# Optimization experiments

Hardware: AMD Instinct MI355X
Metric: run time of the kernel (lower is better)

Reference implementation:

```python
import jax, jax.numpy as jnp
import numpy as np

# Model constants (from Equilibrium3BConfig + hardcoded MambaBlock args)
D_MODEL = 2560
D_INNER = 5120          # expand=2
N_STATE = 128           # d_state
HEADS = 80              # d_inner // headdim
P_HEAD = 64             # headdim
D_CONV = 4
CONV_DIM = D_INNER + 2 * N_STATE        # 5376 (x, B, C share the conv)
D_IN_PROJ = 2 * D_INNER + 2 * N_STATE + HEADS  # 10576 (z, xBC, dt)
N_EXPERTS = 16
TOP_K = 2
M_INTER = 864
MS_INTER = 1728
EPS = 1e-6


def _rms(x, w, eps=EPS):
    xf = x.astype(jnp.float32)
    xf = xf * jax.lax.rsqrt(jnp.mean(xf * xf, axis=-1, keepdims=True) + eps)
    return w * xf.astype(x.dtype)


def setup_inputs() -> dict:
    key = jax.random.key(0)
    ks = jax.random.split(key, 16)
    b, l = 1, 1024
    s = 0.02  # weight scale, keeps activations sane through the deep block
    return {
        "hidden_states": jax.random.normal(ks[0], (b, l, D_MODEL), jnp.float32),
        "w_in": jax.random.normal(ks[1], (D_MODEL, D_IN_PROJ), jnp.float32) * s,
        "conv_w": jax.random.normal(ks[2], (CONV_DIM, D_CONV), jnp.float32) * s,
        "conv_b": jnp.zeros((CONV_DIM,), jnp.float32),
        "dt_bias": jax.random.normal(ks[3], (HEADS,), jnp.float32) * s,
        "A_log": jax.random.normal(ks[4], (HEADS,), jnp.float32) * s,
        "D": jnp.ones((HEADS,), jnp.float32),
        "mamba_norm_w": jnp.ones((D_INNER,), jnp.float32),
        "w_out": jax.random.normal(ks[5], (D_INNER, D_MODEL), jnp.float32) * s,
        "ln1_w": jnp.ones((D_MODEL,), jnp.float32),
        "ln2_w": jnp.ones((D_MODEL,), jnp.float32),
        "router_w": jax.random.normal(ks[6], (D_MODEL, N_EXPERTS), jnp.float32) * s,
        "we_gate": jax.random.normal(ks[7], (N_EXPERTS, D_MODEL, M_INTER), jnp.float32) * s,
        "we_up": jax.random.normal(ks[8], (N_EXPERTS, D_MODEL, M_INTER), jnp.float32) * s,
        "we_down": jax.random.normal(ks[9], (N_EXPERTS, M_INTER, D_MODEL), jnp.float32) * s,
        "ws_gate": jax.random.normal(ks[10], (D_MODEL, MS_INTER), jnp.float32) * s,
        "ws_up": jax.random.normal(ks[11], (D_MODEL, MS_INTER), jnp.float32) * s,
        "ws_down": jax.random.normal(ks[12], (MS_INTER, D_MODEL), jnp.float32) * s,
    }


def _forward(hidden_states, w_in, conv_w, conv_b, dt_bias, A_log, D, mamba_norm_w,
             w_out, ln1_w, ln2_w, router_w, we_gate, we_up, we_down,
             ws_gate, ws_up, ws_down):
    b, l, d = hidden_states.shape

    # ---- Mamba2 (selective scan) sub-block ----
    residual = hidden_states
    x = _rms(hidden_states, ln1_w)
    zxbcdt = x @ w_in  # [b, l, 10576]
    z, xBC, dt = jnp.split(zxbcdt, [D_INNER, D_INNER + CONV_DIM], axis=-1)

    # depthwise causal conv over (x, B, C) channels, then SiLU
    xBC_t = xBC.transpose(0, 2, 1)  # [b, c, l]
    conv = jax.lax.conv_general_dilated(
        xBC_t, conv_w[:, None, :], (1,), [(D_CONV - 1, 0)],
        feature_group_count=CONV_DIM, dimension_numbers=("NCH", "OIH", "NCH"))
    xBC = jax.nn.silu((conv + conv_b[None, :, None]).transpose(0, 2, 1))
    xs, Bc, Cc = jnp.split(xBC, [D_INNER, D_INNER + N_STATE], axis=-1)

    dt = jax.nn.softplus(dt + dt_bias)          # [b, l, h]
    A = -jnp.exp(A_log)                          # [h]
    xh = xs.reshape(b, l, HEADS, P_HEAD)

    # time-major for scan
    dt_l = dt.transpose(1, 0, 2)                 # [l, b, h]
    xh_l = xh.transpose(1, 0, 2, 3)              # [l, b, h, p]
    B_l = Bc.transpose(1, 0, 2)                  # [l, b, n]
    C_l = Cc.transpose(1, 0, 2)                  # [l, b, n]

    def step(h, inp):
        dt_t, x_t, B_t, C_t = inp
        dA = jnp.exp(dt_t * A)                   # [b, h]
        h = h * dA[..., None, None] + (dt_t[..., None] * x_t)[..., None] * B_t[:, None, None, :]
        y = jnp.einsum("bhpn,bn->bhp", h, C_t)
        return h, y

    h0 = jnp.zeros((b, HEADS, P_HEAD, N_STATE), hidden_states.dtype)
    _, y_l = jax.lax.scan(step, h0, (dt_l, xh_l, B_l, C_l))
    y_l = y_l + D[None, None, :, None] * xh_l    # skip term
    y = y_l.transpose(1, 0, 2, 3).reshape(b, l, D_INNER)
    y = _rms(y * jax.nn.silu(z), mamba_norm_w)   # gated RMSNorm
    hidden = residual + y @ w_out

    # ---- DeepSeekMoE sub-block ----
    residual2 = hidden
    xm = _rms(hidden, ln2_w).reshape(b * l, d)
    logits = xm @ router_w
    probs = jax.nn.softmax(logits.astype(jnp.float32), axis=-1)
    topv, topi = jax.lax.top_k(probs, TOP_K)
    topv = topv / jnp.sum(topv, axis=-1, keepdims=True)  # renormalize top-k
    wdense = jnp.sum(jax.nn.one_hot(topi, N_EXPERTS, dtype=xm.dtype)
                     * topv[..., None].astype(xm.dtype), axis=1)  # [T, E]

    # routed experts (SwiGLU), dense-masked faithful math
    hexp = (jax.nn.silu(jnp.einsum("td,edm->tem", xm, we_gate))
            * jnp.einsum("td,edm->tem", xm, we_up))
    y_routed = jnp.einsum("tem,emd,te->td", hexp, we_down, wdense)

    # shared experts (single fused SwiGLU MLP)
    y_shared = (jax.nn.silu(xm @ ws_gate) * (xm @ ws_up)) @ ws_down

    moe = (y_routed + y_shared).reshape(b, l, d)
    return residual2 + moe


def reference(hidden_states, w_in, conv_w, conv_b, dt_bias, A_log, D, mamba_norm_w,
              w_out, ln1_w, ln2_w, router_w, we_gate, we_up, we_down,
              ws_gate, ws_up, ws_down):
    return _forward(hidden_states, w_in, conv_w, conv_b, dt_bias, A_log, D,
                    mamba_norm_w, w_out, ln1_w, ln2_w, router_w,
                    we_gate, we_up, we_down, ws_gate, ws_up, ws_down)
```

## Files before the change

### kernel.cpp

```cpp
#include <hip/hip_runtime.h>

typedef __attribute__((ext_vector_type(4))) float f32x4;
typedef __attribute__((ext_vector_type(8))) __bf16 bf16x8;
typedef __attribute__((ext_vector_type(4))) __bf16 bf16x4;
typedef __attribute__((ext_vector_type(8))) _Float16 f16x8;
typedef __attribute__((ext_vector_type(4))) _Float16 f16x4;

#define D_MODEL 2560
#define D_INNER 5120
#define N_STATE 128
#define HEADS 80
#define P_HEAD 64
#define CONV_DIM 5376
#define D_INPROJ 10576
#define SEQ 1024
#define NCHUNK 16
#define QCHUNK 64
#define NEXP 16
#define M_INTER 864
#define MS_INTER 1728
#define NSLOT 2048
#define NSLOTP 2176

__device__ __forceinline__ float siluf(float x) { return x / (1.f + __expf(-x)); }

__device__ __forceinline__ int swz_p(int k4, int P) {
  return (k4 & ~31) | ((((k4 >> 3) & 3) ^ P) << 3) | (k4 & 7);
}

__device__ __forceinline__ void gl16(const __bf16* g, __bf16* l) {
  __builtin_amdgcn_global_load_lds((const __attribute__((address_space(1))) unsigned int*)g,
                                   (__attribute__((address_space(3))) unsigned int*)l, 16, 0, 0);
}

__device__ __forceinline__ float block_sum256(float v, float* red) {
#pragma unroll
  for (int m = 32; m > 0; m >>= 1) v += __shfl_xor(v, m, 64);
  int w = threadIdx.x >> 6;
  if ((threadIdx.x & 63) == 0) red[w] = v;
  __syncthreads();
  return red[0] + red[1] + red[2] + red[3];
}

template <bool FP16>
__global__ __launch_bounds__(256) void k_rmsnorm_p(const float* __restrict__ in,
                                                   const float* __restrict__ w,
                                                   float* __restrict__ f32out,
                                                   __bf16* __restrict__ ph,
                                                   __bf16* __restrict__ pdh,
                                                   __bf16* __restrict__ pdl, int D) {
  __shared__ float red[4];
  int t = blockIdx.x, tid = threadIdx.x;
  const float* x = in + (size_t)t * D;
  int nd4 = D >> 2;
  float ss = 0.f;
  for (int i = tid; i < nd4; i += 256) {
    float4 v = ((const float4*)x)[i];
    ss += v.x * v.x + v.y * v.y + v.z * v.z + v.w * v.w;
  }
  float tot = block_sum256(ss, red);
  float r = rsqrtf(tot / (float)D + 1e-6f);
  int P = (t >> 1) & 3;
  for (int i = tid; i < nd4; i += 256) {
    float4 v = ((const float4*)x)[i];
    float4 wv = ((const float4*)w)[i];
    float4 o;
    o.x = wv.x * v.x * r; o.y = wv.y * v.y * r; o.z = wv.z * v.z * r; o.w = wv.w * v.w * r;
    if (f32out) ((float4*)(f32out + (size_t)t * D))[i] = o;
    int p = swz_p(i * 4, P);
    if constexpr (FP16) {
      f16x4 hv;
      hv[0] = (_Float16)o.x; hv[1] = (_Float16)o.y; hv[2] = (_Float16)o.z; hv[3] = (_Float16)o.w;
      *(f16x4*)&ph[(size_t)t * D + p] = hv;
    } else {
      bf16x4 hv;
      hv[0] = (__bf16)o.x; hv[1] = (__bf16)o.y; hv[2] = (__bf16)o.z; hv[3] = (__bf16)o.w;
      *(bf16x4*)&ph[(size_t)t * D + p] = hv;
    }
    if (pdh) {
      bf16x4 hv, lv;
      hv[0] = (__bf16)o.x; hv[1] = (__bf16)o.y; hv[2] = (__bf16)o.z; hv[3] = (__bf16)o.w;
      lv[0] = (__bf16)(o.x - (float)hv[0]); lv[1] = (__bf16)(o.y - (float)hv[1]);
      lv[2] = (__bf16)(o.z - (float)hv[2]); lv[3] = (__bf16)(o.w - (float)hv[3]);
      *(bf16x4*)&pdh[(size_t)t * D + p] = hv;
      *(bf16x4*)&pdl[(size_t)t * D + p] = lv;
    }
  }
}

template <bool SPLIT, bool FP16>
__global__ __launch_bounds__(256) void k_transW(const float* __restrict__ W, int ld, int K, int N,
                                                __bf16* __restrict__ Th, __bf16* __restrict__ Tl) {
  __shared__ float T[64][65];
  const int n0 = blockIdx.x * 64, k0 = blockIdx.y * 64, tid = threadIdx.x;
#pragma unroll
  for (int i = 0; i < 16; i++) {
    int idx = tid + i * 256;
    int k = idx >> 6, n = idx & 63;
    float v = 0.f;
    if (n0 + n < N) v = W[(size_t)(k0 + k) * ld + n0 + n];
    T[k][n] = v;
  }
  __syncthreads();
#pragma unroll
  for (int i = 0; i < 4; i++) {
    int idx = tid + i * 256;
    int n = idx >> 4, p4 = (idx & 15) * 4;
    int nn = n0 + n;
    int P = (nn >> 1) & 3;
    if constexpr (SPLIT) {
      bf16x4 hv, lv;
#pragma unroll
      for (int e = 0; e < 4; e++) {
        int p = p4 + e;
        int kk = (p & ~31) | ((((p >> 3) & 3) ^ P) << 3) | (p & 7);
        float v = T[kk][n];
        __bf16 h = (__bf16)v;
        hv[e] = h;
        lv[e] = (__bf16)(v - (float)h);
      }
      *(bf16x4*)&Th[(size_t)nn * K + k0 + p4] = hv;
      *(bf16x4*)&Tl[(size_t)nn * K + k0 + p4] = lv;
    } else if constexpr (FP16) {
      f16x4 hv;
#pragma unroll
      for (int e = 0; e < 4; e++) {
        int p = p4 + e;
        int kk = (p & ~31) | ((((p >> 3) & 3) ^ P) << 3) | (p & 7);
        hv[e] = (_Float16)T[kk][n];
      }
      *(f16x4*)&Th[(size_t)nn * K + k0 + p4] = hv;
    } else {
      bf16x4 hv;
#pragma unroll
      for (int e = 0; e < 4; e++) {
        int p = p4 + e;
        int kk = (p & ~31) | ((((p >> 3) & 3) ^ P) << 3) | (p & 7);
        hv[e] = (__bf16)T[kk][n];
      }
      *(bf16x4*)&Th[(size_t)nn * K + k0 + p4] = hv;
    }
  }
}

template <bool SPLIT, bool FP16>
__global__ __launch_bounds__(256) void k_gemm2(const __bf16* __restrict__ Ah,
                                               const __bf16* __restrict__ Al,
                                               const __bf16* __restrict__ Bh,
                                               const __bf16* __restrict__ Bl,
                                               float* __restrict__ C,
                                               int M, int N, int K, int ks, int nst) {
  constexpr int NP = SPLIT ? 4 : 2;
  __shared__ __bf16 lds[NP * 4096];
  __bf16* const AsH = lds;
  __bf16* const BsH = lds + (SPLIT ? 2 : 1) * 4096;
  __bf16* const AsL = SPLIT ? (lds + 4096) : nullptr;
  __bf16* const BsL = SPLIT ? (lds + 3 * 4096) : nullptr;

  const int tid = threadIdx.x;
  const int T = gridDim.x * gridDim.y * gridDim.z;
  const int linear = blockIdx.x + gridDim.x * (blockIdx.y + gridDim.y * blockIdx.z);
  const int s_idx = (linear & 7) * (T >> 3) + (linear >> 3);
  const int bm = s_idx & 7;
  const int g = s_idx >> 3;
  const int bn = g % gridDim.y;
  const int z = g / gridDim.y;

  const int m0 = bm * 128, n0 = bn * 128;
  const int s0 = (int)(((long long)z * nst) / ks);
  const int s1 = (int)(((long long)(z + 1) * nst) / ks);
  float* __restrict__ Cp = C + (size_t)z * M * N;

  const int lane = tid & 63, wid = tid >> 6;
  const int wr = wid >> 1, wc = wid & 1;
  const int l16 = lane & 15, kl = lane >> 4;

  const int srow = tid >> 2;
  const int schunk = (tid & 3) * 8;
  const size_t aB0 = (size_t)(m0 + srow) * K + schunk;
  const size_t aB1 = aB0 + (size_t)64 * K;
  const size_t bB0 = (size_t)(n0 + srow) * K + schunk;
  const size_t bB1 = bB0 + (size_t)64 * K;
  __bf16* const lA0 = AsH + tid * 8;
  __bf16* const lA1 = AsH + (tid + 256) * 8;
  __bf16* const lB0 = BsH + tid * 8;
  __bf16* const lB1 = BsH + (tid + 256) * 8;

  int aoff[4], boff[4];
#pragma unroll
  for (int mi = 0; mi < 4; mi++) {
    int r = wr * 64 + mi * 16 + l16;
    aoff[mi] = r * 64 + ((kl ^ ((r >> 1) & 3)) << 4);
  }
#pragma unroll
  for (int ni = 0; ni < 4; ni++) {
    int r = wc * 64 + ni * 16 + l16;
    boff[ni] = r * 64 + ((kl ^ ((r >> 1) & 3)) << 4);
  }

  f32x4 acc[4][4];
#pragma unroll
  for (int mi = 0; mi < 4; mi++)
#pragma unroll
    for (int ni = 0; ni < 4; ni++) acc[mi][ni] = f32x4{0.f, 0.f, 0.f, 0.f};

  for (int s = s0; s < s1; ++s) {
    const int k0 = s << 5;
    __syncthreads();
    gl16(Ah + aB0 + k0, lA0);
    gl16(Ah + aB1 + k0, lA1);
    gl16(Bh + bB0 + k0, lB0);
    gl16(Bh + bB1 + k0, lB1);
    if constexpr (SPLIT) {
      gl16(Al + aB0 + k0, AsL + tid * 8);
      gl16(Al + aB1 + k0, AsL + (tid + 256) * 8);
      gl16(Bl + bB0 + k0, BsL + tid * 8);
      gl16(Bl + bB1 + k0, BsL + (tid + 256) * 8);
    }
    __syncthreads();
    if constexpr (!SPLIT && FP16) {
      f16x8 ah[4], bh[4];
#pragma unroll
      for (int mi = 0; mi < 4; mi++) ah[mi] = *(const f16x8*)((const char*)AsH + aoff[mi]);
#pragma unroll
      for (int ni = 0; ni < 4; ni++) bh[ni] = *(const f16x8*)((const char*)BsH + boff[ni]);
#pragma unroll
      for (int mi = 0; mi < 4; mi++)
#pragma unroll
        for (int ni = 0; ni < 4; ni++)
          acc[mi][ni] = __builtin_amdgcn_mfma_f32_16x16x32_f16(ah[mi], bh[ni], acc[mi][ni], 0, 0, 0);
    } else {
      bf16x8 ah[4], bh[4];
#pragma unroll
      for (int mi = 0; mi < 4; mi++) ah[mi] = *(const bf16x8*)((const char*)AsH + aoff[mi]);
#pragma unroll
      for (int ni = 0; ni < 4; ni++) bh[ni] = *(const bf16x8*)((const char*)BsH + boff[ni]);
#pragma unroll
      for (int mi = 0; mi < 4; mi++)
#pragma unroll
        for (int ni = 0; ni < 4; ni++)
          acc[mi][ni] = __builtin_amdgcn_mfma_f32_16x16x32_bf16(ah[mi], bh[ni], acc[mi][ni], 0, 0, 0);
      if constexpr (SPLIT) {
        bf16x8 al[4], bl[4];
#pragma unroll
        for (int mi = 0; mi < 4; mi++) al[mi] = *(const bf16x8*)((const char*)AsL + aoff[mi]);
#pragma unroll
        for (int ni = 0; ni < 4; ni++) bl[ni] = *(const bf16x8*)((const char*)BsL + boff[ni]);
#pragma unroll
        for (int mi = 0; mi < 4; mi++)
#pragma unroll
          for (int ni = 0; ni < 4; ni++) {
            acc[mi][ni] = __builtin_amdgcn_mfma_f32_16x16x32_bf16(ah[mi], bl[ni], acc[mi][ni], 0, 0, 0);
            acc[mi][ni] = __builtin_amdgcn_mfma_f32_16x16x32_bf16(al[mi], bh[ni], acc[mi][ni], 0, 0, 0);
          }
      }
    }
  }
#pragma unroll
  for (int mi = 0; mi < 4; mi++)
#pragma unroll
    for (int ni = 0; ni < 4; ni++)
#pragma unroll
      for (int r = 0; r < 4; r++) {
        int row = m0 + wr * 64 + mi * 16 + kl * 4 + r;
        int col = n0 + wc * 64 + ni * 16 + l16;
        if (col < N) Cp[(size_t)row * N + col] = acc[mi][ni][r];
      }
}

template <bool RES>
__global__ void k_reduce(const float* __restrict__ Pp, int np, int n4,
                         const float* __restrict__ res, float* __restrict__ out) {
  int i = blockIdx.x * 256 + threadIdx.x;
  int stride = gridDim.x * 256;
  for (; i < n4; i += stride) {
    float4 a = ((const float4*)Pp)[i];
    for (int z = 1; z < np; z++) {
      float4 b = ((const float4*)Pp)[(size_t)z * n4 + i];
      a.x += b.x; a.y += b.y; a.z += b.z; a.w += b.w;
    }
    if constexpr (RES) {
      float4 r0 = ((const float4*)res)[i];
      a.x += r0.x; a.y += r0.y; a.z += r0.z; a.w += r0.w;
    }
    ((float4*)out)[i] = a;
  }
}

__global__ void k_dtfin(const float* __restrict__ dtP, const float* __restrict__ dt_bias,
                        const float* __restrict__ A_log, float* __restrict__ dtp,
                        float* __restrict__ dtA) {
  int t = blockIdx.x, h = threadIdx.x;
  if (h < HEADS) {
    float v = dt_bias[h];
#pragma unroll
    for (int z = 0; z < 8; z++) v += dtP[((size_t)z * SEQ + t) * 80 + h];
    float sp = fmaxf(v, 0.f) + log1pf(expf(-fabsf(v)));
    dtp[t * HEADS + h] = sp;
    dtA[t * HEADS + h] = sp * (-expf(A_log[h]));
  }
}

__global__ __launch_bounds__(256) void k_gatherA(const float* __restrict__ xm,
                                                 const int* __restrict__ perm,
                                                 __bf16* __restrict__ Aslots) {
  int s = blockIdx.x, tid = threadIdx.x;
  int t = perm[s];
// ... 98 lines not shown
      if (more) {
#pragma unroll
        for (int e4 = 0; e4 < 4; e4++) {
          bf16x4 h;
          h[0] = (__bf16)nv[0][e4]; h[1] = (__bf16)nv[1][e4];
          h[2] = (__bf16)nv[2][e4]; h[3] = (__bf16)nv[3][e4];
          *(bf16x4*)&Bsl[cur ^ 1][cb * 4 + e4][kb * 4] = h;
        }
      }
      __syncthreads();
      cur ^= 1;
    }
#pragma unroll
    for (int mi = 0; mi < 4; mi++)
#pragma unroll
      for (int ni = 0; ni < 4; ni++)
#pragma unroll
        for (int r = 0; r < 4; r++) {
          int rl = bm * 128 + wr * 64 + mi * 16 + kl * 4 + r;
          int col = n0 + wc * 64 + ni * 16 + l16;
          if (rl < cnt && col < N) Cpl[(size_t)(base + rl) * N + col] = acc[mi][ni][r];
        }
  }
}

__global__ __launch_bounds__(256) void k_silumulE(const float* __restrict__ gP,
                                                  const float* __restrict__ uP,
                                                  const float* __restrict__ slotw,
                                                  __bf16* __restrict__ outp) {
  int s = blockIdx.x, tid = threadIdx.x;
  float w = slotw[s];
  int P = (s >> 1) & 3;
  const size_t PL = (size_t)NSLOTP * M_INTER;
  for (int i = tid; i < M_INTER / 4; i += 256) {
    f32x4 g = f32x4{0.f, 0.f, 0.f, 0.f}, u = f32x4{0.f, 0.f, 0.f, 0.f};
#pragma unroll
    for (int z = 0; z < 4; z++) {
      g += *(const f32x4*)&gP[z * PL + (size_t)s * M_INTER + i * 4];
      u += *(const f32x4*)&uP[z * PL + (size_t)s * M_INTER + i * 4];
    }
    int p = swz_p(i * 4, P);
    bf16x4 h;
    h[0] = (__bf16)(siluf(g[0]) * u[0] * w);
    h[1] = (__bf16)(siluf(g[1]) * u[1] * w);
    h[2] = (__bf16)(siluf(g[2]) * u[2] * w);
    h[3] = (__bf16)(siluf(g[3]) * u[3] * w);
    *(bf16x4*)&outp[(size_t)s * M_INTER + p] = h;
  }
}

__global__ __launch_bounds__(256) void k_silumul_sh2(const float* __restrict__ P4,
                                                     __bf16* __restrict__ outp) {
  int t = blockIdx.x, tid = threadIdx.x;
  int P = (t >> 1) & 3;
  const size_t PL = (size_t)SEQ * 3456;
  for (int i = tid; i < MS_INTER / 4; i += 256) {
    f32x4 g = f32x4{0.f, 0.f, 0.f, 0.f}, u = f32x4{0.f, 0.f, 0.f, 0.f};
#pragma unroll
    for (int z = 0; z < 4; z++) {
      g += *(const f32x4*)&P4[z * PL + (size_t)t * 3456 + i * 4];
      u += *(const f32x4*)&P4[z * PL + (size_t)t * 3456 + 1728 + i * 4];
    }
    int p = swz_p(i * 4, P);
    bf16x4 h;
    h[0] = (__bf16)(siluf(g[0]) * u[0]);
    h[1] = (__bf16)(siluf(g[1]) * u[1]);
    h[2] = (__bf16)(siluf(g[2]) * u[2]);
    h[3] = (__bf16)(siluf(g[3]) * u[3]);
    *(bf16x4*)&outp[(size_t)t * MS_INTER + p] = h;
  }
}

__global__ void k_conv(const float* __restrict__ zx, const float* __restrict__ cw,
                       const float* __restrict__ cb, float* __restrict__ xBC) {
  int cidx = blockIdx.x * 256 + threadIdx.x;
  int t = blockIdx.y;
  if (cidx < CONV_DIM) {
    float acc = cb[cidx];
#pragma unroll
    for (int j = 0; j < 4; j++) {
      int tt = t - 3 + j;
      if (tt >= 0) acc += zx[(size_t)tt * D_INPROJ + D_INNER + cidx] * cw[cidx * 4 + j];
    }
    xBC[(size_t)t * CONV_DIM + cidx] = siluf(acc);
  }
}

__global__ __launch_bounds__(256) void k_scan_intra(
    const float* __restrict__ xBC, const float* __restrict__ dtp,
    const float* __restrict__ dtA, float* __restrict__ y, float* __restrict__ S,
    float* __restrict__ cumA, float* __restrict__ Atot) {
  __shared__ float Bs[64][132];
  __shared__ float Cs[64][132];
  __shared__ float Xs[64][68];
  __shared__ float Gs[64][65];
  __shared__ float da_s[64], a_s[64], dt_sh[64], w_sh[64];
  int c = blockIdx.x, h = blockIdx.y, tid = threadIdx.x;
  int t0 = c * QCHUNK;
#pragma unroll
  for (int i = 0; i < 8; i++) {
    int id = tid + 256 * i;
    int r = id >> 5, c4 = (id & 31) * 4;
    *(float4*)&Bs[r][c4] = *(const float4*)&xBC[(size_t)(t0 + r) * CONV_DIM + D_INNER + c4];
    *(float4*)&Cs[r][c4] = *(const float4*)&xBC[(size_t)(t0 + r) * CONV_DIM + D_INNER + N_STATE + c4];
  }
#pragma unroll
  for (int i = 0; i < 4; i++) {
    int id = tid + 256 * i;
    int r = id >> 4, p4 = (id & 15) * 4;
    *(float4*)&Xs[r][p4] = *(const float4*)&xBC[(size_t)(t0 + r) * CONV_DIM + h * P_HEAD + p4];
  }
  if (tid < 64) {
    da_s[tid] = dtA[(size_t)(t0 + tid) * HEADS + h];
    dt_sh[tid] = dtp[(size_t)(t0 + tid) * HEADS + h];
  }
  __syncthreads();
  if (tid < 64) {
    float a = 0.f;
    for (int i = 0; i <= tid; i++) a += da_s[i];
    a_s[tid] = a;
    cumA[((size_t)c * HEADS + h) * 64 + tid] = a;
  }
  __syncthreads();
  if (tid < 64) {
    w_sh[tid] = __expf(a_s[63] - a_s[tid]) * dt_sh[tid];
    if (tid == 0) Atot[c * HEADS + h] = a_s[63];
  }
  __syncthreads();
  {
    int tq = tid >> 4, sq = tid & 15;
    float gacc[4][4];
#pragma unroll
    for (int j = 0; j < 4; j++)
#pragma unroll
      for (int jj = 0; jj < 4; jj++) gacc[j][jj] = 0.f;
// ... 75 lines not shown
__global__ __launch_bounds__(256) void k_scan_inter(
    const float* __restrict__ xBC, const float* __restrict__ Hin,
    const float* __restrict__ cumA, const float* __restrict__ Dv,
    float* __restrict__ y) {
  __shared__ float Hs[64][132];
  __shared__ float Cs[64][132];
  __shared__ float a_l[64];
  int c = blockIdx.x, h = blockIdx.y, tid = threadIdx.x;
  int t0 = c * QCHUNK;
#pragma unroll
  for (int i = 0; i < 8; i++) {
    int id = tid + 256 * i;
    int r = id >> 5, n4 = (id & 31) * 4;
    *(float4*)&Hs[r][n4] = *(const float4*)&Hin[(((size_t)(c * HEADS + h) * 64 + r) << 7) + n4];
    *(float4*)&Cs[r][n4] = *(const float4*)&xBC[(size_t)(t0 + r) * CONV_DIM + D_INNER + N_STATE + n4];
  }
  if (tid < 64) a_l[tid] = cumA[((size_t)c * HEADS + h) * 64 + tid];
  __syncthreads();
  float Dh = Dv[h];
  int tq = tid >> 4, pq = tid & 15;
  float4 acc[4];
#pragma unroll
  for (int j = 0; j < 4; j++) acc[j] = float4{0.f, 0.f, 0.f, 0.f};
  for (int n4 = 0; n4 < 128; n4 += 4) {
    float4 hv[4], cv[4];
#pragma unroll
    for (int jj = 0; jj < 4; jj++) hv[jj] = *(const float4*)&Hs[pq * 4 + jj][n4];
#pragma unroll
    for (int j = 0; j < 4; j++) cv[j] = *(const float4*)&Cs[tq * 4 + j][n4];
#pragma unroll
    for (int j = 0; j < 4; j++) {
      acc[j].x += cv[j].x * hv[0].x + cv[j].y * hv[0].y + cv[j].z * hv[0].z + cv[j].w * hv[0].w;
      acc[j].y += cv[j].x * hv[1].x + cv[j].y * hv[1].y + cv[j].z * hv[1].z + cv[j].w * hv[1].w;
      acc[j].z += cv[j].x * hv[2].x + cv[j].y * hv[2].y + cv[j].z * hv[2].z + cv[j].w * hv[2].w;
      acc[j].w += cv[j].x * hv[3].x + cv[j].y * hv[3].y + cv[j].z * hv[3].z + cv[j].w * hv[3].w;
    }
  }
#pragma unroll
  for (int j = 0; j < 4; j++) {
    int t = tq * 4 + j;
    float e = __expf(a_l[t]);
    float4 xv = *(const float4*)&xBC[(size_t)(t0 + t) * CONV_DIM + h * P_HEAD + pq * 4];
    size_t yoff = (size_t)(t0 + t) * D_INNER + h * P_HEAD + pq * 4;
    float4 yv = *(float4*)&y[yoff];
    yv.x += e * acc[j].x + Dh * xv.x;
    yv.y += e * acc[j].y + Dh * xv.y;
    yv.z += e * acc[j].z + Dh * xv.z;
    yv.w += e * acc[j].w + Dh * xv.w;
    *(float4*)&y[yoff] = yv;
  }
}

__global__ __launch_bounds__(256) void k_gatednorm_p(const float* __restrict__ y,
                                                     const float* __restrict__ zx,
                                                     const float* __restrict__ w,
                                                     __bf16* __restrict__ ph) {
  __shared__ float vbuf[D_INNER];
  __shared__ float red[4];
  int t = blockIdx.x, tid = threadIdx.x;
  float ss = 0.f;
  for (int i = tid; i < D_INNER / 4; i += 256) {
    float4 yv = *(const float4*)&y[(size_t)t * D_INNER + i * 4];
    float4 zv = *(const float4*)&zx[(size_t)t * D_INPROJ + i * 4];
    float4 v;
    v.x = yv.x * siluf(zv.x); v.y = yv.y * siluf(zv.y);
    v.z = yv.z * siluf(zv.z); v.w = yv.w * siluf(zv.w);
    *(float4*)&vbuf[i * 4] = v;
    ss += v.x * v.x + v.y * v.y + v.z * v.z + v.w * v.w;
  }
  float tot = block_sum256(ss, red);
  float r = rsqrtf(tot / (float)D_INNER + 1e-6f);
  int P = (t >> 1) & 3;
  for (int i = tid; i < D_INNER / 4; i += 256) {
    float4 v = *(const float4*)&vbuf[i * 4];
    float4 wv = *(const float4*)&w[i * 4];
    float4 o;
    o.x = wv.x * v.x * r; o.y = wv.y * v.y * r; o.z = wv.z * v.z * r; o.w = wv.w * v.w * r;
    int p = swz_p(i * 4, P);
    f16x4 hv;
    hv[0] = (_Float16)o.x; hv[1] = (_Float16)o.y; hv[2] = (_Float16)o.z; hv[3] = (_Float16)o.w;
    *(f16x4*)&ph[(size_t)t * D_INNER + p] = hv;
  }
}

__global__ void k_zero(int* counts, int* cursor) {
  int i = threadIdx.x;
  if (i < NEXP) { counts[i] = 0; cursor[i] = 0; }
}

__global__ __launch_bounds__(256) void k_router(const float* __restrict__ xm,
                                                const float* __restrict__ Wr,
                                                int* __restrict__ top_i,
                                                float* __restrict__ top_v,
                                                int* __restrict__ counts) {
  __shared__ float part[16][17];
  __shared__ float lg[16];
  int t = blockIdx.x, tid = threadIdx.x;
  int e = tid & 15, seg = tid >> 4;
  const float* xr = xm + (size_t)t * D_MODEL;
  float s = 0.f;
  for (int i = 0; i < 160; i++) {
    int k = seg * 160 + i;
    s += xr[k] * Wr[(size_t)k * NEXP + e];
  }
  part[seg][e] = s;
  __syncthreads();
  if (tid < 16) {
    float l = 0.f;
    for (int g = 0; g < 16; g++) l += part[g][tid];
    lg[tid] = l;
  }
  __syncthreads();
  if (tid == 0) {
    float mx = lg[0];
    for (int i = 1; i < 16; i++) mx = fmaxf(mx, lg[i]);
    float pe[16];
    for (int i = 0; i < 16; i++) pe[i] = expf(lg[i] - mx);
    int i0 = 0; float v0 = pe[0];
    for (int i = 1; i < 16; i++) if (pe[i] > v0) { v0 = pe[i]; i0 = i; }
    int i1 = -1; float v1 = -1.f;
    for (int i = 0; i < 16; i++) if (i != i0 && pe[i] > v1) { v1 = pe[i]; i1 = i; }
    float inv = 1.f / (v0 + v1);
    top_i[t * 2] = i0; top_i[t * 2 + 1] = i1;
    top_v[t * 2] = v0 * inv; top_v[t * 2 + 1] = v1 * inv;
    atomicAdd(&counts[i0], 1);
    atomicAdd(&counts[i1], 1);
  }
}

__global__ void k_offsets(const int* counts, int* offs, int* cursor) {
  if (threadIdx.x == 0) {
// ... 16 lines not shown
    }
  }
}

__global__ void k_final2(const float* __restrict__ hidden, const float* __restrict__ sh,
                         const float* __restrict__ dsP, const int* __restrict__ slotOf,
                         float* __restrict__ out) {
  int t = blockIdx.y;
  int d4 = (blockIdx.x * 256 + threadIdx.x) * 4;
  if (d4 < D_MODEL) {
    int s0 = slotOf[t * 2], s1 = slotOf[t * 2 + 1];
    f32x4 a = *(const f32x4*)&hidden[(size_t)t * D_MODEL + d4];
    f32x4 b = *(const f32x4*)&sh[(size_t)t * D_MODEL + d4];
    f32x4 acc = a + b;
    const size_t PL = (size_t)NSLOTP * D_MODEL;
#pragma unroll
    for (int z = 0; z < 3; z++) {
      acc += *(const f32x4*)&dsP[z * PL + (size_t)s0 * D_MODEL + d4];
      acc += *(const f32x4*)&dsP[z * PL + (size_t)s1 * D_MODEL + d4];
    }
    *(f32x4*)&out[(size_t)t * D_MODEL + d4] = acc;
  }
}

extern "C" void kernel_launch(void* const* d_in, const int* in_sizes, int n_in,
                              void* d_out, int out_size, void* d_ws, size_t ws_size,
                              hipStream_t stream) {
  const float* hs = (const float*)d_in[0];
  const float* w_in = (const float*)d_in[1];
  const float* conv_w = (const float*)d_in[2];
  const float* conv_b = (const float*)d_in[3];
  const float* dt_bias = (const float*)d_in[4];
  const float* A_log = (const float*)d_in[5];
  const float* Dv = (const float*)d_in[6];
  const float* mnw = (const float*)d_in[7];
  const float* w_out = (const float*)d_in[8];
  const float* ln1 = (const float*)d_in[9];
  const float* ln2 = (const float*)d_in[10];
  const float* router_w = (const float*)d_in[11];
  const float* we_gate = (const float*)d_in[12];
  const float* we_up = (const float*)d_in[13];
  const float* we_down = (const float*)d_in[14];
  const float* ws_gate = (const float*)d_in[15];
  const float* ws_up = (const float*)d_in[16];
  const float* ws_down = (const float*)d_in[17];

  char* base = (char*)d_ws;
  size_t off = 0;
  auto A = [&](size_t bytes) -> void* {
    void* p = base + off;
    off += (bytes + 255) & ~(size_t)255;
    return p;
  };
  float* zx = (float*)A((size_t)SEQ * D_INPROJ * 4);
  float* xbc = (float*)A((size_t)SEQ * CONV_DIM * 4);
  float* xmf = (float*)A((size_t)SEQ * D_MODEL * 4);
  float* dtp = (float*)A((size_t)SEQ * HEADS * 4);
  float* dtA = (float*)A((size_t)SEQ * HEADS * 4);
  float* yf = (float*)A((size_t)SEQ * D_INNER * 4);
  float* cumA = (float*)A((size_t)NCHUNK * HEADS * 64 * 4);
  float* Atot = (float*)A((size_t)NCHUNK * HEADS * 4);
  float* Sbuf = (float*)A((size_t)NCHUNK * HEADS * 64 * 128 * 4);
  float* hidden = (float*)A((size_t)SEQ * D_MODEL * 4);
  float* shout = (float*)A((size_t)SEQ * D_MODEL * 4);
  float* top_v = (float*)A(8192);
  float* slotw = (float*)A(8192);
  int* top_i = (int*)A(8192);
  int* counts = (int*)A(64);
  int* offs = (int*)A(64);
  int* cursor = (int*)A(64);
  int* perm = (int*)A(8192);
  int* slotOf = (int*)A(8192);
  __bf16* xp_h = (__bf16*)A((size_t)SEQ * D_MODEL * 2);
  __bf16* ybp_h = (__bf16*)A((size_t)SEQ * D_INNER * 2);
  __bf16* gbuf_bh = (__bf16*)A((size_t)SEQ * MS_INTER * 2);
  char* REG = (char*)A((size_t)146000000);

  __bf16* winT_h = (__bf16*)REG;
  __bf16* woutT_h = (__bf16*)REG;
  float* partials = (float*)(REG + 60000000);
  __bf16* xdt_h = (__bf16*)(REG + 110000000);
  __bf16* xdt_l = (__bf16*)(REG + 115500000);
  __bf16* wdt_h = (__bf16*)(REG + 121000000);
  __bf16* wdt_l = (__bf16*)(REG + 122000000);
  float* dtP = (float*)(REG + 123000000);
  __bf16* guT = (__bf16*)REG;
  __bf16* downT = (__bf16*)(REG + 18350080);
  float* partials4 = (float*)(REG + 30000000);
  __bf16* Aslots = (__bf16*)REG;
  __bf16* gsl = (__bf16*)(REG + 12000000);
  float* gateP = (float*)(REG + 16000000);
  float* upP = (float*)(REG + 47000000);
  float* dslotsP = (float*)(REG + 78000000);

  k_rmsnorm_p<true><<<SEQ, 256, 0, stream>>>(hs, ln1, nullptr, xp_h, xdt_h, xdt_l, D_MODEL);
  k_transW<false, true><<<dim3(166, 40), 256, 0, stream>>>(w_in, D_INPROJ, D_MODEL, D_INPROJ,
                                                           winT_h, nullptr);
  k_transW<true, false><<<dim3(2, 40), 256, 0, stream>>>(w_in + 10496, D_INPROJ, D_MODEL, 80,
                                                         wdt_h, wdt_l);
  k_gemm2<false, true><<<dim3(8, 83, 1), 256, 0, stream>>>(xp_h, nullptr, winT_h, nullptr, zx,
                                                           SEQ, D_INPROJ, D_MODEL, 1, 80);
  k_gemm2<true, false><<<dim3(8, 1, 8), 256, 0, stream>>>(xdt_h, xdt_l, wdt_h, wdt_l, dtP,
                                                          SEQ, 80, D_MODEL, 8, 80);
  k_dtfin<<<SEQ, 128, 0, stream>>>(dtP, dt_bias, A_log, dtp, dtA);
  k_conv<<<dim3(21, SEQ), 256, 0, stream>>>(zx, conv_w, conv_b, xbc);
  k_scan_intra<<<dim3(NCHUNK, HEADS), 256, 0, stream>>>(xbc, dtp, dtA, yf, Sbuf, cumA, Atot);
  k_scan_state<<<2560, 256, 0, stream>>>(Sbuf, Atot);
  k_scan_inter<<<dim3(NCHUNK, HEADS), 256, 0, stream>>>(xbc, Sbuf, cumA, Dv, yf);
  k_gatednorm_p<<<SEQ, 256, 0, stream>>>(yf, zx, mnw, ybp_h);
  k_transW<false, true><<<dim3(40, 80), 256, 0, stream>>>(w_out, D_MODEL, D_INNER, D_MODEL,
                                                          woutT_h, nullptr);
  k_gemm2<false, true><<<dim3(8, 20, 4), 256, 0, stream>>>(ybp_h, nullptr, woutT_h, nullptr,
                                                           partials, SEQ, D_MODEL, D_INNER, 4, 160);
  k_reduce<true><<<2048, 256, 0, stream>>>(partials, 4, SEQ * D_MODEL / 4, hs, hidden);

  k_rmsnorm_p<false><<<SEQ, 256, 0, stream>>>(hidden, ln2, xmf, xp_h, nullptr, nullptr, D_MODEL);
  k_zero<<<1, 64, 0, stream>>>(counts, cursor);
  k_router<<<SEQ, 256, 0, stream>>>(xmf, router_w, top_i, top_v, counts);
  k_offsets<<<1, 32, 0, stream>>>(counts, offs, cursor);
  k_scatter<<<4, 256, 0, stream>>>(top_i, top_v, cursor, perm, slotOf, slotw);

  k_transW<false, false><<<dim3(27, 40), 256, 0, stream>>>(ws_gate, MS_INTER, D_MODEL, MS_INTER,
                                                           guT, nullptr);
  k_transW<false, false><<<dim3(27, 40), 256, 0, stream>>>(ws_up, MS_INTER, D_MODEL, MS_INTER,
                                                           guT + (size_t)MS_INTER * D_MODEL, nullptr);
  k_gemm2<false, false><<<dim3(8, 27, 4), 256, 0, stream>>>(xp_h, nullptr, guT, nullptr, partials4,
                                                            SEQ, 3456, D_MODEL, 4, 80);
  k_silumul_sh2<<<SEQ, 256, 0, stream>>>(partials4, gbuf_bh);
  k_transW<false, false><<<dim3(40, 27), 256, 0, stream>>>(ws_down, D_MODEL, MS_INTER, D_MODEL,
                                                           downT, nullptr);
  k_gemm2<false, false><<<dim3(8, 20, 4), 256, 0, stream>>>(gbuf_bh, nullptr, downT, nullptr,
                                                            partials4, SEQ, D_MODEL, MS_INTER, 4, 54);
  k_reduce<false><<<2048, 256, 0, stream>>>(partials4, 4, SEQ * D_MODEL / 4, nullptr, shout);

  k_gatherA<<<NSLOT, 256, 0, stream>>>(xmf, perm, Aslots);
  k_gemmE2<4><<<dim3(7, 4, NEXP), 256, 0, stream>>>(Aslots, we_gate, gateP, offs, counts,
                                                    M_INTER, D_MODEL, (long long)D_MODEL * M_INTER);
  k_gemmE2<4><<<dim3(7, 4, NEXP), 256, 0, stream>>>(Aslots, we_up, upP, offs, counts,
                                                    M_INTER, D_MODEL, (long long)D_MODEL * M_INTER);
  k_silumulE<<<NSLOT, 256, 0, stream>>>(gateP, upP, slotw, gsl);
  k_gemmE2<3><<<dim3(20, 3, NEXP), 256, 0, stream>>>(gsl, we_down, dslotsP, offs, counts,
                                                     D_MODEL, M_INTER, (long long)M_INTER * D_MODEL);

  k_final2<<<dim3(3, SEQ), 256, 0, stream>>>(hidden, shout, dslotsP, slotOf, (float*)d_out);
}
```

Baseline: 845.7 us.

## Use BK=64 GEMM tiles with 8-way swizzle and split-K the in-projection

```diff
diff --git a/kernel.cpp b/kernel.cpp
--- a/kernel.cpp
+++ b/kernel.cpp
@@ -27,6 +27,9 @@
 __device__ __forceinline__ int swz_p(int k4, int P) {
   return (k4 & ~31) | ((((k4 >> 3) & 3) ^ P) << 3) | (k4 & 7);
 }
+__device__ __forceinline__ int swz64(int k4, int row) {
+  return (k4 & ~63) | (((((k4 >> 3) & 7) ^ (row & 7)) << 3)) | (k4 & 7);
+}
 
 __device__ __forceinline__ void gl16(const __bf16* g, __bf16* l) {
   __builtin_amdgcn_global_load_lds((const __attribute__((address_space(1))) unsigned int*)g,
@@ -67,17 +70,18 @@
     float4 o;
     o.x = wv.x * v.x * r; o.y = wv.y * v.y * r; o.z = wv.z * v.z * r; o.w = wv.w * v.w * r;
     if (f32out) ((float4*)(f32out + (size_t)t * D))[i] = o;
-    int p = swz_p(i * 4, P);
+    int p64 = swz64(i * 4, t);
     if constexpr (FP16) {
       f16x4 hv;
       hv[0] = (_Float16)o.x; hv[1] = (_Float16)o.y; hv[2] = (_Float16)o.z; hv[3] = (_Float16)o.w;
-      *(f16x4*)&ph[(size_t)t * D + p] = hv;
+      *(f16x4*)&ph[(size_t)t * D + p64] = hv;
     } else {
       bf16x4 hv;
       hv[0] = (__bf16)o.x; hv[1] = (__bf16)o.y; hv[2] = (__bf16)o.z; hv[3] = (__bf16)o.w;
-      *(bf16x4*)&ph[(size_t)t * D + p] = hv;
+      *(bf16x4*)&ph[(size_t)t * D + p64] = hv;
     }
     if (pdh) {
+      int p = swz_p(i * 4, P);
       bf16x4 hv, lv;
       hv[0] = (__bf16)o.x; hv[1] = (__bf16)o.y; hv[2] = (__bf16)o.z; hv[3] = (__bf16)o.w;
       lv[0] = (__bf16)(o.x - (float)hv[0]); lv[1] = (__bf16)(o.y - (float)hv[1]);
@@ -107,8 +111,8 @@
     int idx = tid + i * 256;
     int n = idx >> 4, p4 = (idx & 15) * 4;
     int nn = n0 + n;
-    int P = (nn >> 1) & 3;
     if constexpr (SPLIT) {
+      int P = (nn >> 1) & 3;
       bf16x4 hv, lv;
 #pragma unroll
       for (int e = 0; e < 4; e++) {
@@ -126,7 +130,7 @@
 #pragma unroll
       for (int e = 0; e < 4; e++) {
         int p = p4 + e;
-        int kk = (p & ~31) | ((((p >> 3) & 3) ^ P) << 3) | (p & 7);
+        int kk = swz64(p, nn);
         hv[e] = (_Float16)T[kk][n];
       }
       *(f16x4*)&Th[(size_t)nn * K + k0 + p4] = hv;
@@ -135,7 +139,7 @@
 #pragma unroll
       for (int e = 0; e < 4; e++) {
         int p = p4 + e;
-        int kk = (p & ~31) | ((((p >> 3) & 3) ^ P) << 3) | (p & 7);
+        int kk = swz64(p, nn);
         hv[e] = (__bf16)T[kk][n];
       }
       *(bf16x4*)&Th[(size_t)nn * K + k0 + p4] = hv;
@@ -143,19 +147,24 @@
   }
 }
 
-template <bool SPLIT, bool FP16>
+template <bool SPLIT, bool FP16, int BK>
 __global__ __launch_bounds__(256) void k_gemm2(const __bf16* __restrict__ Ah,
                                                const __bf16* __restrict__ Al,
                                                const __bf16* __restrict__ Bh,
                                                const __bf16* __restrict__ Bl,
                                                float* __restrict__ C,
                                                int M, int N, int K, int ks, int nst) {
-  constexpr int NP = SPLIT ? 4 : 2;
-  __shared__ __bf16 lds[NP * 4096];
+  constexpr int PLE = 128 * BK;
+  constexpr int NPL = SPLIT ? 4 : 2;
+  constexpr int CALLS = PLE / 2048;
+  constexpr int CPR = BK / 8;
+  constexpr int RPC = 256 / CPR;
+  constexpr int KSUB = BK / 32;
+  __shared__ __bf16 lds[NPL * PLE];
   __bf16* const AsH = lds;
-  __bf16* const BsH = lds + (SPLIT ? 2 : 1) * 4096;
-  __bf16* const AsL = SPLIT ? (lds + 4096) : nullptr;
-  __bf16* const BsL = SPLIT ? (lds + 3 * 4096) : nullptr;
+  __bf16* const BsH = lds + (SPLIT ? 2 : 1) * PLE;
+  __bf16* const AsL = SPLIT ? (lds + PLE) : nullptr;
+  __bf16* const BsL = SPLIT ? (lds + 3 * PLE) : nullptr;
 
   const int tid = threadIdx.x;
   const int T = gridDim.x * gridDim.y * gridDim.z;
@@ -175,27 +184,30 @@
   const int wr = wid >> 1, wc = wid & 1;
   const int l16 = lane & 15, kl = lane >> 4;
 
-  const int srow = tid >> 2;
-  const int schunk = (tid & 3) * 8;
-  const size_t aB0 = (size_t)(m0 + srow) * K + schunk;
-  const size_t aB1 = aB0 + (size_t)64 * K;
-  const size_t bB0 = (size_t)(n0 + srow) * K + schunk;
-  const size_t bB1 = bB0 + (size_t)64 * K;
-  __bf16* const lA0 = AsH + tid * 8;
-  __bf16* const lA1 = AsH + (tid + 256) * 8;
-  __bf16* const lB0 = BsH + tid * 8;
-  __bf16* const lB1 = BsH + (tid + 256) * 8;
-
-  int aoff[4], boff[4];
+  const int srow = tid / CPR;
+  const int schunk = (tid % CPR) * 8;
+  size_t aB[CALLS], bB[CALLS];
+#pragma unroll
+  for (int i = 0; i < CALLS; i++) {
+    aB[i] = (size_t)(m0 + srow + RPC * i) * K + schunk;
+    bB[i] = (size_t)(n0 + srow + RPC * i) * K + schunk;
+  }
+
+  int aoff[4][KSUB], boff[4][KSUB];
 #pragma unroll
   for (int mi = 0; mi < 4; mi++) {
-    int r = wr * 64 + mi * 16 + l16;
-    aoff[mi] = r * 64 + ((kl ^ ((r >> 1) & 3)) << 4);
-  }
-#pragma unroll
-  for (int ni = 0; ni < 4; ni++) {
-    int r = wc * 64 + ni * 16 + l16;
-    boff[ni] = r * 64 + ((kl ^ ((r >> 1) & 3)) << 4);
+    int ra = wr * 64 + mi * 16 + l16;
+    int rb = wc * 64 + mi * 16 + l16;
+#pragma unroll
+    for (int kk = 0; kk < KSUB; kk++) {
+      if constexpr (BK == 32) {
+        aoff[mi][kk] = ra * 64 + ((kl ^ ((ra >> 1) & 3)) << 4);
+        boff[mi][kk] = rb * 64 + ((kl ^ ((rb >> 1) & 3)) << 4);
+      } else {
+        aoff[mi][kk] = ra * (2 * BK) + (((kk * 4 + kl) ^ (ra & 7)) << 4);
+        boff[mi][kk] = rb * (2 * BK) + (((kk * 4 + kl) ^ (rb & 7)) << 4);
+      }
+    }
   }
 
   f32x4 acc[4][4];
@@ -205,54 +217,56 @@
     for (int ni = 0; ni < 4; ni++) acc[mi][ni] = f32x4{0.f, 0.f, 0.f, 0.f};
 
   for (int s = s0; s < s1; ++s) {
-    const int k0 = s << 5;
+    const int kof = s * BK;
     __syncthreads();
-    gl16(Ah + aB0 + k0, lA0);
-    gl16(Ah + aB1 + k0, lA1);
-    gl16(Bh + bB0 + k0, lB0);
-    gl16(Bh + bB1 + k0, lB1);
-    if constexpr (SPLIT) {
-      gl16(Al + aB0 + k0, AsL + tid * 8);
-      gl16(Al + aB1 + k0, AsL + (tid + 256) * 8);
-      gl16(Bl + bB0 + k0, BsL + tid * 8);
-      gl16(Bl + bB1 + k0, BsL + (tid + 256) * 8);
+#pragma unroll
+    for (int i = 0; i < CALLS; i++) {
+      gl16(Ah + aB[i] + kof, AsH + (tid + i * 256) * 8);
+      gl16(Bh + bB[i] + kof, BsH + (tid + i * 256) * 8);
+      if constexpr (SPLIT) {
+        gl16(Al + aB[i] + kof, AsL + (tid + i * 256) * 8);
+        gl16(Bl + bB[i] + kof, BsL + (tid + i * 256) * 8);
+      }
     }
     __syncthreads();
-    if constexpr (!SPLIT && FP16) {
-      f16x8 ah[4], bh[4];
-#pragma unroll
-      for (int mi = 0; mi < 4; mi++) ah[mi] = *(const f16x8*)((const char*)AsH + aoff[mi]);
-#pragma unroll
-      for (int ni = 0; ni < 4; ni++) bh[ni] = *(const f16x8*)((const char*)BsH + boff[ni]);
-#pragma unroll
-      for (int mi = 0; mi < 4; mi++)
-#pragma unroll
-        for (int ni = 0; ni < 4; ni++)
-          acc[mi][ni] = __builtin_amdgcn_mfma_f32_16x16x32_f16(ah[mi], bh[ni], acc[mi][ni], 0, 0, 0);
-    } else {
-      bf16x8 ah[4], bh[4];
-#pragma unroll
-      for (int mi = 0; mi < 4; mi++) ah[mi] = *(const bf16x8*)((const char*)AsH + aoff[mi]);
-#pragma unroll
-      for (int ni = 0; ni < 4; ni++) bh[ni] = *(const bf16x8*)((const char*)BsH + boff[ni]);
-#pragma unroll
-      for (int mi = 0; mi < 4; mi++)
-#pragma unroll
-        for (int ni = 0; ni < 4; ni++)
-          acc[mi][ni] = __builtin_amdgcn_mfma_f32_16x16x32_bf16(ah[mi], bh[ni], acc[mi][ni], 0, 0, 0);
-      if constexpr (SPLIT) {
-        bf16x8 al[4], bl[4];
-#pragma unroll
-        for (int mi = 0; mi < 4; mi++) al[mi] = *(const bf16x8*)((const char*)AsL + aoff[mi]);
-#pragma unroll
-        for (int ni = 0; ni < 4; ni++) bl[ni] = *(const bf16x8*)((const char*)BsL + boff[ni]);
+#pragma unroll
+    for (int kk = 0; kk < KSUB; kk++) {
+      if constexpr (!SPLIT && FP16) {
+        f16x8 ah[4], bh[4];
+#pragma unroll
+        for (int mi = 0; mi < 4; mi++) ah[mi] = *(const f16x8*)((const char*)AsH + aoff[mi][kk]);
+#pragma unroll
+        for (int ni = 0; ni < 4; ni++) bh[ni] = *(const f16x8*)((const char*)BsH + boff[ni][kk]);
 #pragma unroll
         for (int mi = 0; mi < 4; mi++)
 #pragma unroll
-          for (int ni = 0; ni < 4; ni++) {
-            acc[mi][ni] = __builtin_amdgcn_mfma_f32_16x16x32_bf16(ah[mi], bl[ni], acc[mi][ni], 0, 0, 0);
-            acc[mi][ni] = __builtin_amdgcn_mfma_f32_16x16x32_bf16(al[mi], bh[ni], acc[mi][ni], 0, 0, 0);
-          }
+          for (int ni = 0; ni < 4; ni++)
+            acc[mi][ni] = __builtin_amdgcn_mfma_f32_16x16x32_f16(ah[mi], bh[ni], acc[mi][ni], 0, 0, 0);
+      } else {
+        bf16x8 ah[4], bh[4];
+#pragma unroll
+        for (int mi = 0; mi < 4; mi++) ah[mi] = *(const bf16x8*)((const char*)AsH + aoff[mi][kk]);
+#pragma unroll
+        for (int ni = 0; ni < 4; ni++) bh[ni] = *(const bf16x8*)((const char*)BsH + boff[ni][kk]);
+#pragma unroll
+        for (int mi = 0; mi < 4; mi++)
+#pragma unroll
+          for (int ni = 0; ni < 4; ni++)
+            acc[mi][ni] = __builtin_amdgcn_mfma_f32_16x16x32_bf16(ah[mi], bh[ni], acc[mi][ni], 0, 0, 0);
+        if constexpr (SPLIT) {
+          bf16x8 al[4], bl[4];
+#pragma unroll
+          for (int mi = 0; mi < 4; mi++) al[mi] = *(const bf16x8*)((const char*)AsL + aoff[mi][kk]);
+#pragma unroll
+          for (int ni = 0; ni < 4; ni++) bl[ni] = *(const bf16x8*)((const char*)BsL + boff[ni][kk]);
+#pragma unroll
+          for (int mi = 0; mi < 4; mi++)
+#pragma unroll
+            for (int ni = 0; ni < 4; ni++) {
+              acc[mi][ni] = __builtin_amdgcn_mfma_f32_16x16x32_bf16(ah[mi], bl[ni], acc[mi][ni], 0, 0, 0);
+              acc[mi][ni] = __builtin_amdgcn_mfma_f32_16x16x32_bf16(al[mi], bh[ni], acc[mi][ni], 0, 0, 0);
+            }
+        }
       }
     }
   }
@@ -457,7 +471,6 @@
 __global__ __launch_bounds__(256) void k_silumul_sh2(const float* __restrict__ P4,
                                                      __bf16* __restrict__ outp) {
   int t = blockIdx.x, tid = threadIdx.x;
-  int P = (t >> 1) & 3;
   const size_t PL = (size_t)SEQ * 3456;
   for (int i = tid; i < MS_INTER / 4; i += 256) {
     f32x4 g = f32x4{0.f, 0.f, 0.f, 0.f}, u = f32x4{0.f, 0.f, 0.f, 0.f};
@@ -466,7 +479,7 @@
       g += *(const f32x4*)&P4[z * PL + (size_t)t * 3456 + i * 4];
       u += *(const f32x4*)&P4[z * PL + (size_t)t * 3456 + 1728 + i * 4];
     }
-    int p = swz_p(i * 4, P);
+    int p = swz64(i * 4, t);
     bf16x4 h;
     h[0] = (__bf16)(siluf(g[0]) * u[0]);
     h[1] = (__bf16)(siluf(g[1]) * u[1]);
@@ -476,8 +489,9 @@
   }
 }
 
-__global__ void k_conv(const float* __restrict__ zx, const float* __restrict__ cw,
-                       const float* __restrict__ cb, float* __restrict__ xBC) {
+__global__ void k_conv(const float* __restrict__ zx0, const float* __restrict__ zx1,
+                       const float* __restrict__ cw, const float* __restrict__ cb,
+                       float* __restrict__ xBC) {
   int cidx = blockIdx.x * 256 + threadIdx.x;
   int t = blockIdx.y;
   if (cidx < CONV_DIM) {
@@ -485,7 +499,10 @@
 #pragma unroll
     for (int j = 0; j < 4; j++) {
       int tt = t - 3 + j;
-      if (tt >= 0) acc += zx[(size_t)tt * D_INPROJ + D_INNER + cidx] * cw[cidx * 4 + j];
+      if (tt >= 0) {
+        size_t idx = (size_t)tt * D_INPROJ + D_INNER + cidx;
+        acc += (zx0[idx] + zx1[idx]) * cw[cidx * 4 + j];
+      }
     }
     xBC[(size_t)t * CONV_DIM + cidx] = siluf(acc);
   }
@@ -667,7 +684,8 @@
 }
 
 __global__ __launch_bounds__(256) void k_gatednorm_p(const float* __restrict__ y,
-                                                     const float* __restrict__ zx,
+                                                     const float* __restrict__ zx0,
+                                                     const float* __restrict__ zx1,
                                                      const float* __restrict__ w,
                                                      __bf16* __restrict__ ph) {
   __shared__ float vbuf[D_INNER];
@@ -676,22 +694,23 @@
   float ss = 0.f;
   for (int i = tid; i < D_INNER / 4; i += 256) {
     float4 yv = *(const float4*)&y[(size_t)t * D_INNER + i * 4];
-    float4 zv = *(const float4*)&zx[(size_t)t * D_INPROJ + i * 4];
+    f32x4 z0 = *(const f32x4*)&zx0[(size_t)t * D_INPROJ + i * 4];
+    f32x4 z1 = *(const f32x4*)&zx1[(size_t)t * D_INPROJ + i * 4];
+    f32x4 zs = z0 + z1;
     float4 v;
-    v.x = yv.x * siluf(zv.x); v.y = yv.y * siluf(zv.y);
-    v.z = yv.z * siluf(zv.z); v.w = yv.w * siluf(zv.w);
+    v.x = yv.x * siluf(zs[0]); v.y = yv.y * siluf(zs[1]);
+    v.z = yv.z * siluf(zs[2]); v.w = yv.w * siluf(zs[3]);
     *(float4*)&vbuf[i * 4] = v;
     ss += v.x * v.x + v.y * v.y + v.z * v.z + v.w * v.w;
   }
   float tot = block_sum256(ss, red);
   float r = rsqrtf(tot / (float)D_INNER + 1e-6f);
-  int P = (t >> 1) & 3;
   for (int i = tid; i < D_INNER / 4; i += 256) {
     float4 v = *(const float4*)&vbuf[i * 4];
     float4 wv = *(const float4*)&w[i * 4];
     float4 o;
     o.x = wv.x * v.x * r; o.y = wv.y * v.y * r; o.z = wv.z * v.z * r; o.w = wv.w * v.w * r;
-    int p = swz_p(i * 4, P);
+    int p = swz64(i * 4, t);
     f16x4 hv;
     hv[0] = (_Float16)o.x; hv[1] = (_Float16)o.y; hv[2] = (_Float16)o.z; hv[3] = (_Float16)o.w;
     *(f16x4*)&ph[(size_t)t * D_INNER + p] = hv;
@@ -814,7 +833,6 @@
     off += (bytes + 255) & ~(size_t)255;
     return p;
   };
-  float* zx = (float*)A((size_t)SEQ * D_INPROJ * 4);
   float* xbc = (float*)A((size_t)SEQ * CONV_DIM * 4);
   float* xmf = (float*)A((size_t)SEQ * D_MODEL * 4);
   float* dtp = (float*)A((size_t)SEQ * HEADS * 4);
@@ -836,16 +854,18 @@
   __bf16* xp_h = (__bf16*)A((size_t)SEQ * D_MODEL * 2);
   __bf16* ybp_h = (__bf16*)A((size_t)SEQ * D_INNER * 2);
   __bf16* gbuf_bh = (__bf16*)A((size_t)SEQ * MS_INTER * 2);
-  char* REG = (char*)A((size_t)146000000);
+  char* REG = (char*)A((size_t)163000000);
 
   __bf16* winT_h = (__bf16*)REG;
+  float* zxP = (float*)(REG + 60000000);
+  const size_t ZXPL = (size_t)SEQ * D_INPROJ;
+  __bf16* xdt_h = (__bf16*)(REG + 147000000);
+  __bf16* xdt_l = (__bf16*)(REG + 152500000);
+  __bf16* wdt_h = (__bf16*)(REG + 158000000);
+  __bf16* wdt_l = (__bf16*)(REG + 158700000);
+  float* dtP = (float*)(REG + 159400000);
   __bf16* woutT_h = (__bf16*)REG;
   float* partials = (float*)(REG + 60000000);
-  __bf16* xdt_h = (__bf16*)(REG + 110000000);
-  __bf16* xdt_l = (__bf16*)(REG + 115500000);
-  __bf16* wdt_h = (__bf16*)(REG + 121000000);
-  __bf16* wdt_l = (__bf16*)(REG + 122000000);
-  float* dtP = (float*)(REG + 123000000);
   __bf16* guT = (__bf16*)REG;
   __bf16* downT = (__bf16*)(REG + 18350080);
   float* partials4 = (float*)(REG + 30000000);
@@ -860,20 +880,20 @@
                                                            winT_h, nullptr);
   k_transW<true, false><<<dim3(2, 40), 256, 0, stream>>>(w_in + 10496, D_INPROJ, D_MODEL, 80,
                                                          wdt_h, wdt_l);
-  k_gemm2<false, true><<<dim3(8, 83, 1), 256, 0, stream>>>(xp_h, nullptr, winT_h, nullptr, zx,
-                                                           SEQ, D_INPROJ, D_MODEL, 1, 80);
-  k_gemm2<true, false><<<dim3(8, 1, 8), 256, 0, stream>>>(xdt_h, xdt_l, wdt_h, wdt_l, dtP,
-                                                          SEQ, 80, D_MODEL, 8, 80);
+  k_gemm2<false, true, 64><<<dim3(8, 83, 2), 256, 0, stream>>>(xp_h, nullptr, winT_h, nullptr, zxP,
+                                                               SEQ, D_INPROJ, D_MODEL, 2, 40);
+  k_gemm2<true, false, 32><<<dim3(8, 1, 8), 256, 0, stream>>>(xdt_h, xdt_l, wdt_h, wdt_l, dtP,
+                                                              SEQ, 80, D_MODEL, 8, 80);
   k_dtfin<<<SEQ, 128, 0, stream>>>(dtP, dt_bias, A_log, dtp, dtA);
-  k_conv<<<dim3(21, SEQ), 256, 0, stream>>>(zx, conv_w, conv_b, xbc);
+  k_conv<<<dim3(21, SEQ), 256, 0, stream>>>(zxP, zxP + ZXPL, conv_w, conv_b, xbc);
   k_scan_intra<<<dim3(NCHUNK, HEADS), 256, 0, stream>>>(xbc, dtp, dtA, yf, Sbuf, cumA, Atot);
   k_scan_state<<<2560, 256, 0, stream>>>(Sbuf, Atot);
   k_scan_inter<<<dim3(NCHUNK, HEADS), 256, 0, stream>>>(xbc, Sbuf, cumA, Dv, yf);
-  k_gatednorm_p<<<SEQ, 256, 0, stream>>>(yf, zx, mnw, ybp_h);
+  k_gatednorm_p<<<SEQ, 256, 0, stream>>>(yf, zxP, zxP + ZXPL, mnw, ybp_h);
   k_transW<false, true><<<dim3(40, 80), 256, 0, stream>>>(w_out, D_MODEL, D_INNER, D_MODEL,
                                                           woutT_h, nullptr);
-  k_gemm2<false, true><<<dim3(8, 20, 4), 256, 0, stream>>>(ybp_h, nullptr, woutT_h, nullptr,
-                                                           partials, SEQ, D_MODEL, D_INNER, 4, 160);
+  k_gemm2<false, true, 64><<<dim3(8, 20, 4), 256, 0, stream>>>(ybp_h, nullptr, woutT_h, nullptr,
+                                                               partials, SEQ, D_MODEL, D_INNER, 4, 80);
   k_reduce<true><<<2048, 256, 0, stream>>>(partials, 4, SEQ * D_MODEL / 4, hs, hidden);
 
   k_rmsnorm_p<false><<<SEQ, 256, 0, stream>>>(hidden, ln2, xmf, xp_h, nullptr, nullptr, D_MODEL);
@@ -886,13 +906,13 @@
                                                            guT, nullptr);
   k_transW<false, false><<<dim3(27, 40), 256, 0, stream>>>(ws_up, MS_INTER, D_MODEL, MS_INTER,
                                                            guT + (size_t)MS_INTER * D_MODEL, nullptr);
-  k_gemm2<false, false><<<dim3(8, 27, 4), 256, 0, stream>>>(xp_h, nullptr, guT, nullptr, partials4,
-                                                            SEQ, 3456, D_MODEL, 4, 80);
+  k_gemm2<false, false, 64><<<dim3(8, 27, 4), 256, 0, stream>>>(xp_h, nullptr, guT, nullptr,
+                                                                partials4, SEQ, 3456, D_MODEL, 4, 40);
   k_silumul_sh2<<<SEQ, 256, 0, stream>>>(partials4, gbuf_bh);
   k_transW<false, false><<<dim3(40, 27), 256, 0, stream>>>(ws_down, D_MODEL, MS_INTER, D_MODEL,
                                                            downT, nullptr);
-  k_gemm2<false, false><<<dim3(8, 20, 4), 256, 0, stream>>>(gbuf_bh, nullptr, downT, nullptr,
-                                                            partials4, SEQ, D_MODEL, MS_INTER, 4, 54);
+  k_gemm2<false, false, 64><<<dim3(8, 20, 4), 256, 0, stream>>>(gbuf_bh, nullptr, downT, nullptr,
+                                                                partials4, SEQ, D_MODEL, MS_INTER, 4, 27);
   k_reduce<false><<<2048, 256, 0, stream>>>(partials4, 4, SEQ * D_MODEL / 4, nullptr, shout);
 
   k_gatherA<<<NSLOT, 256, 0, stream>>>(xmf, perm, Aslots);
```

New measurement: 850.6 us. Within noise of the previous version (+0.6%).
